# Optimization experiments

Measured on AMD Instinct MI355X. Metric: run time of the kernel, lower is better.

The kernel has to match this reference:

```python
import jax, jax.numpy as jnp
import numpy as np

B, S, D, A, C, TT, T, NS = 64, 512, 1024, 128, 64, 32, 40, 64
NEG = -1e9


def setup_inputs() -> dict:
    key = jax.random.key(0)
    ks = jax.random.split(key, 24)
    n = lambda k, sh, s: jax.random.normal(k, sh, dtype=jnp.float32) * s
    inp = {
        "encoded_src": n(ks[0], (B, S, D), 1.0),
        "encoded_col": n(ks[1], (B, C, D), 1.0),
        "encoded_tab": n(ks[2], (B, TT, D), 1.0),
        "h0": n(ks[3], (B, D), 1.0),
        "c0": n(ks[4], (B, D), 1.0),
        "action_emb": n(ks[5], (A, D), 0.1),
        "symbol_emb": n(ks[6], (NS, D), 0.1),
        "W_tgt": n(ks[7], (D, D), 0.02), "b_tgt": jnp.zeros((D,), jnp.float32),
        "W_act": n(ks[8], (D, D), 0.02), "b_act": jnp.zeros((D,), jnp.float32),
        "W_col": n(ks[9], (D, D), 0.02), "b_col": jnp.zeros((D,), jnp.float32),
        "W_tab": n(ks[10], (D, D), 0.02), "b_tab": jnp.zeros((D,), jnp.float32),
        "W_out": n(ks[11], (D, D), 0.02), "b_out": jnp.zeros((D,), jnp.float32),
        "W_ih": n(ks[12], (3 * D, 4 * D), 0.02), "b_ih": jnp.zeros((4 * D,), jnp.float32),
        "W_hh": n(ks[13], (D, 4 * D), 0.02), "b_hh": jnp.zeros((4 * D,), jnp.float32),
        "src_mask": jnp.zeros((B, S), jnp.int32),
        "col_mask": jnp.zeros((B, C), jnp.int32),
        "tab_mask": jnp.zeros((B, TT), jnp.int32),
        "action_mask": jnp.zeros((B, A), jnp.int32),
        "cur_node_ids": jax.random.randint(ks[14], (T, B), 0, NS, dtype=jnp.int32),
        "kind": jax.random.randint(ks[15], (T, B), 0, 3, dtype=jnp.int32),
        "gold_idx": jax.random.randint(ks[16], (T, B), 0, TT, dtype=jnp.int32),
    }
    return inp


def reference(encoded_src, encoded_col, encoded_tab, h0, c0, action_emb, symbol_emb,
              W_tgt, b_tgt, W_act, b_act, W_col, b_col, W_tab, b_tab, W_out, b_out,
              W_ih, b_ih, W_hh, b_hh,
              src_mask, col_mask, tab_mask, action_mask, cur_node_ids, kind, gold_idx):
    dt = encoded_src.dtype
    nT, nB = cur_node_ids.shape
    nA = action_emb.shape[0]
    nC = encoded_col.shape[1]
    nTT = encoded_tab.shape[1]
    dim = encoded_src.shape[-1]

    # mask==1 means masked-out (matches torch code: allowed positions set to 0)
    src_bias = jnp.where(src_mask == 1, NEG, 0.0).astype(dt)
    act_bias = jnp.where(action_mask == 1, NEG, 0.0).astype(dt)
    col_bias = jnp.where(col_mask == 1, NEG, 0.0).astype(dt)
    tab_bias = jnp.where(tab_mask == 1, NEG, 0.0).astype(dt)

    # previous-action embedding per step: gather from action table / encoded cols / encoded tabs
    bidx = jnp.arange(nB)
    prev_a = action_emb[gold_idx % nA]                       # [T,B,D]
    prev_c = encoded_col[bidx[None, :], gold_idx % nC]       # [T,B,D]
    prev_t = encoded_tab[bidx[None, :], gold_idx % nTT]      # [T,B,D]
    k3 = kind[..., None]
    prev_sel = jnp.where(k3 == 0, prev_a, jnp.where(k3 == 1, prev_c, prev_t))
    # step 0 uses a zero prev-action embedding
    prev_emb = jnp.concatenate([jnp.zeros((1, nB, dim), dt), prev_sel[:-1]], axis=0)
    node_emb = symbol_emb[cur_node_ids]                      # [T,B,D]

    def step(carry, xs):
        h, c, loss = carry
        pe, ne, kd, gi = xs
        # attention over encoded_src using affine(h) as query
        q = h @ W_tgt + b_tgt                                            # [B,D]
        att = jax.nn.softmax(jnp.einsum('bsd,bd->bs', encoded_src, q) + src_bias, axis=-1)
        ctx = jnp.einsum('bs,bsd->bd', att, encoded_src)                 # [B,D]
        # LSTMCell
        x = jnp.concatenate([pe, ne, ctx], axis=-1)                      # [B,3D]
        gates = x @ W_ih + b_ih + h @ W_hh + b_hh                        # [B,4D]
        i, f, g, o = jnp.split(gates, 4, axis=-1)
        c2 = jax.nn.sigmoid(f) * c + jax.nn.sigmoid(i) * jnp.tanh(g)
        h2 = jax.nn.sigmoid(o) * jnp.tanh(c2)
        out = h2 @ W_out + b_out                                         # [B,D]
        # three prediction heads (action / column / table views)
        la = jax.nn.log_softmax(jnp.einsum('ad,bd->ba', action_emb, out @ W_act + b_act) + act_bias, axis=-1)
        lc = jax.nn.log_softmax(jnp.einsum('bcd,bd->bc', encoded_col, out @ W_col + b_col) + col_bias, axis=-1)
        lt = jax.nn.log_softmax(jnp.einsum('btd,bd->bt', encoded_tab, out @ W_tab + b_tab) + tab_bias, axis=-1)
        ga = jnp.take_along_axis(la, (gi % nA)[:, None], 1)[:, 0]
        gc = jnp.take_along_axis(lc, (gi % nC)[:, None], 1)[:, 0]
        gt = jnp.take_along_axis(lt, (gi % nTT)[:, None], 1)[:, 0]
        lp = jnp.where(kd == 0, ga, jnp.where(kd == 1, gc, gt))
        return (h2, c2, loss - lp), None

    (h, c, loss), _ = jax.lax.scan(step, (h0, c0, jnp.zeros((nB,), dt)),
                                   (prev_emb, node_emb, kind, gold_idx))
    return loss
```

## Files before the change

kernel.cpp:

```cpp
#include <hip/hip_runtime.h>
#include <math.h>

typedef short s8v __attribute__((ext_vector_type(8)));
typedef __bf16 bf8 __attribute__((ext_vector_type(8)));
typedef float f4v __attribute__((ext_vector_type(4)));

#define DEV static __device__ __forceinline__

DEV ushort f2bf(float f){
  union { float f; unsigned u; } v; v.f = f;
  unsigned u = v.u;
  return (ushort)((u + 0x7fffu + ((u>>16)&1u)) >> 16);
}
DEV float bf2f(ushort u){
  union { unsigned u; float f; } v; v.u = ((unsigned)u)<<16; return v.f;
}
DEV float sigm(float x){ return 1.0f/(1.0f + __expf(-x)); }
DEV float tanh_(float x){ float e=__expf(2.f*x); return 1.f - 2.f/(e+1.f); }
DEV float wred(float x){
  #pragma unroll
  for(int off=32; off; off>>=1) x += __shfl_xor(x, off, 64);
  return x;
}
DEV int swz(int row, int uscol){
  return (row<<6) + ((((uscol>>3) ^ (row&7))<<3) | (uscol&7));
}
DEV void gload16(const void* g, void* l){
  __builtin_amdgcn_global_load_lds((const __attribute__((address_space(1))) void*)g,
                                   (__attribute__((address_space(3))) void*)l, 16, 0, 0);
}
DEV int gperm(int n){
  return (((n&1023)>>4)<<6) | ((n>>10)<<4) | (n&15);
}


__global__ void k_cast(const float* __restrict__ s, ushort* __restrict__ d, long n4){
  long i = (long)blockIdx.x*256 + threadIdx.x;
  const long st = (long)gridDim.x*256;
  for(; i<n4; i+=st){
    float4 v = ((const float4*)s)[i];
    ushort4 o; o.x=f2bf(v.x); o.y=f2bf(v.y); o.z=f2bf(v.z); o.w=f2bf(v.w);
    ((ushort4*)d)[i]=o;
  }
}

__global__ __launch_bounds__(256) void k_tr7(const float* __restrict__ wih,
    const float* __restrict__ whh, const float* __restrict__ wtgt,
    const float* __restrict__ wcol, const float* __restrict__ wtab,
    const float* __restrict__ wact, ushort* __restrict__ WihT,
    ushort* __restrict__ WcatT, ushort* __restrict__ WtgtT, ushort* __restrict__ BcatT)
{
  __shared__ ushort T[64][72];
  const int bid = blockIdx.x;
  const float* src; ushort* dst; int C, ldd, roff, cx, ry; bool pm;
  if(bid < 2048){ src=wih; C=4096; dst=WihT; ldd=2048; roff=0; cx=bid&63; ry=bid>>6; pm=true; }
  else if(bid < 3072){ int j=bid-2048; src=wih+2048L*4096; C=4096; dst=WcatT; ldd=2048; roff=0; cx=j&63; ry=j>>6; pm=true; }
  else if(bid < 4096){ int j=bid-3072; src=whh; C=4096; dst=WcatT; ldd=2048; roff=1024; cx=j&63; ry=j>>6; pm=true; }
  else if(bid < 4352){ int j=bid-4096; src=wtgt; C=1024; dst=WtgtT; ldd=1024; roff=0; cx=j&15; ry=j>>4; pm=false; }
  else if(bid < 4608){ int j=bid-4352; src=wcol; C=1024; dst=BcatT; ldd=1024; roff=0; cx=j&15; ry=j>>4; pm=false; }
  else if(bid < 4864){ int j=bid-4608; src=wtab; C=1024; dst=BcatT+1048576; ldd=1024; roff=0; cx=j&15; ry=j>>4; pm=false; }
  else { int j=bid-4864; src=wact; C=1024; dst=BcatT+2097152; ldd=1024; roff=0; cx=j&15; ry=j>>4; pm=false; }
  const int c0 = cx<<6, r0 = ry<<6;
  const int tid = threadIdx.x;
  {
    const int rr = tid>>2, cc = (tid&3)<<4;
    const float* s = src + (long)(r0+rr)*C + c0 + cc;
    float4 v0=*(const float4*)(s), v1=*(const float4*)(s+4), v2=*(const float4*)(s+8), v3=*(const float4*)(s+12);
    ushort* t = &T[rr][cc];
    t[0]=f2bf(v0.x); t[1]=f2bf(v0.y); t[2]=f2bf(v0.z); t[3]=f2bf(v0.w);
    t[4]=f2bf(v1.x); t[5]=f2bf(v1.y); t[6]=f2bf(v1.z); t[7]=f2bf(v1.w);
    t[8]=f2bf(v2.x); t[9]=f2bf(v2.y); t[10]=f2bf(v2.z); t[11]=f2bf(v2.w);
    t[12]=f2bf(v3.x); t[13]=f2bf(v3.y); t[14]=f2bf(v3.z); t[15]=f2bf(v3.w);
  }
  __syncthreads();
  {
    const int rr = tid>>2, cc = (tid&3)<<4;
    s8v o0, o1;
    #pragma unroll
    for(int i=0;i<8;i++){ o0[i]=(short)T[cc+i][rr]; o1[i]=(short)T[cc+8+i][rr]; }
    const int n = c0 + rr;
    const int nr = pm ? gperm(n) : n;
    ushort* dp = dst + (long)nr*ldd + roff + r0 + cc;
    *(s8v*)dp = o0; *(s8v*)(dp+8) = o1;
  }
}

__global__ void k_gatherP(const float* __restrict__ emba, const float* __restrict__ ecol,
                          const float* __restrict__ etab, const float* __restrict__ symb,
                          const int* __restrict__ kindv, const int* __restrict__ gold,
                          const int* __restrict__ cur, ushort* __restrict__ P){
  long i = (long)blockIdx.x*256 + threadIdx.x;
  const long st = (long)gridDim.x*256;
  const long n4 = 2560L*2048/4;
  for(; i<n4; i+=st){
    long pos = i*4; int row = (int)(pos>>11); int col = (int)(pos&2047);
    int t = row>>6, b = row&63;
    ushort4 o;
    if(col < 1024){
      if(t==0){ o.x=o.y=o.z=o.w=0; *(ushort4*)&P[pos]=o; continue; }
      int k = kindv[(t-1)*64+b];
      int gi = gold[(t-1)*64+b];
      const float* s;
      if(k==0) s = emba + ((long)(gi & 127))*1024 + col;
      else if(k==1) s = ecol + (((long)b<<6) + (gi & 63))*1024 + col;
      else s = etab + (((long)b<<5) + (gi & 31))*1024 + col;
      float4 v = *(const float4*)s;
      o.x=f2bf(v.x); o.y=f2bf(v.y); o.z=f2bf(v.z); o.w=f2bf(v.w);
    } else {
      const float* s = symb + ((long)cur[t*64+b])*1024 + (col-1024);
      float4 v = *(const float4*)s;
      o.x=f2bf(v.x); o.y=f2bf(v.y); o.z=f2bf(v.z); o.w=f2bf(v.w);
    }
    *(ushort4*)&P[pos] = o;
  }
}

__global__ void k_init(const float* __restrict__ h0, const float* __restrict__ c0,
                       const float* __restrict__ bih, const float* __restrict__ bhh,
                       const int* __restrict__ smask,
                       float* __restrict__ cbuf, ushort* __restrict__ Ab0,
                       float* __restrict__ biasvec, float* __restrict__ sbias){
  int i = blockIdx.x*256 + threadIdx.x;
  if(i < 65536){
    cbuf[i]=c0[i];
    int row=i>>10, col=i&1023;
    Ab0[(row<<11)+1024+col]=f2bf(h0[i]);
  }
  if(i < 32768) sbias[i] = (smask[i]==1) ? -1.0e9f : 0.f;
  if(i < 4096){
    int nt=i>>6, g=(i>>4)&3, j16=i&15;
    int n = (g<<10) | (nt<<4) | j16;
    biasvec[i] = bih[n] + bhh[n];
  }
}

__global__ __launch_bounds__(256) void k_bias1b(const float* __restrict__ bout,
    const ushort* __restrict__ BcatT, const float* __restrict__ ba,
    const float* __restrict__ bc, const float* __restrict__ bt,
    float* __restrict__ vv)
{
  const int wid = blockIdx.x*4 + (threadIdx.x>>6);
  const int l = threadIdx.x & 63;
  const int which = wid>>10, col = wid&1023;
  const ushort* W = (which==0) ? (BcatT + 2097152)
                  : (which==1) ? BcatT
                               : (BcatT + 1048576);
  const float bb = ((which==0)?ba:(which==1)?bc:bt)[col];
  const ushort* wp = W + (long)col*1024 + l*16;
  const float* bp = bout + l*16;
  s8v w0 = *(const s8v*)wp, w1 = *(const s8v*)(wp+8);
  float s = 0.f;
  #pragma unroll
  for(int i=0;i<8;i++){
    s += bf2f((ushort)w0[i]) * bp[i];
    s += bf2f((ushort)w1[i]) * bp[8+i];
  }
  s = wred(s);
  if(l==0) vv[wid] = bb + s;
}

__global__ void k_bias2a(const float* __restrict__ vv, const float* __restrict__ emb,
                         const float* __restrict__ ecol, const float* __restrict__ etab,
                         float* __restrict__ dbuf){
  int wid = blockIdx.x*4 + (threadIdx.x>>6);
  int l = threadIdx.x & 63;
  if(wid >= 6272) return;
  const float* src; const float* v;
  if(wid < 128){ src = emb + ((long)wid<<10); v = vv; }
  else if(wid < 4224){ src = ecol + ((long)(wid-128)<<10); v = vv+1024; }
  else { src = etab + ((long)(wid-4224)<<10); v = vv+2048; }
  const float* sp = src + l*16; const float* vp = v + l*16;
  float s = 0.f;
  #pragma unroll
  for(int i=0;i<16;i+=4){
    float4 a = *(const float4*)(sp+i); float4 bvv = *(const float4*)(vp+i);
    s += a.x*bvv.x + a.y*bvv.y + a.z*bvv.z + a.w*bvv.w;
  }
  s = wred(s);
  if(l==0) dbuf[wid] = s;
}

__global__ void k_bias2b(const float* __restrict__ dbuf,
                         const int* __restrict__ amask, const int* __restrict__ cmask,
                         const int* __restrict__ tmask,
                         float* __restrict__ ca, float* __restrict__ cb, float* __restrict__ ct){
  int i = blockIdx.x*256 + threadIdx.x;
  if(i < 8192){ ca[i] = dbuf[i&127] + ((amask[i]==1)?-1.0e9f:0.f); }
  else if(i < 12288){ int j=i-8192; cb[j] = dbuf[128+j] + ((cmask[j]==1)?-1.0e9f:0.f); }
  else if(i < 14336){ int j=i-12288; ct[j] = dbuf[4224+j] + ((tmask[j]==1)?-1.0e9f:0.f); }
}

template<bool OBF16, bool HASB>
__global__ __launch_bounds__(256,2) void k_gemm128(const ushort* __restrict__ Ap,
    const ushort* __restrict__ Bp, void* __restrict__ Cp, const float* __restrict__ bias,
    int N, int K)
{
  __shared__ __align__(16) ushort As[2][8192];
  __shared__ __align__(16) ushort Bs[2][8192];
  const int tid=threadIdx.x, w=tid>>6, l=tid&63;
  const int wr=w>>1, wc=w&1;
  const int m0=blockIdx.y<<7, n0=blockIdx.x<<7;
  const int lr8 = l>>3, lc = l&7;
  f4v acc[4][4];
  #pragma unroll
  for(int m=0;m<4;m++)
    #pragma unroll
    for(int n=0;n<4;n++) acc[m][n]=(f4v){0.f,0.f,0.f,0.f};

  auto stage=[&](int buf, int k0){
    #pragma unroll
    for(int i=0;i<4;i++){
      const int rb = i*32 + w*8;
      const int row = rb + lr8;
      const int cp = (lc ^ (row&7))<<3;
      gload16(Ap + (long)(m0+row)*K + k0 + cp, &As[buf][rb<<6]);
      gload16(Bp + (long)(n0+row)*K + k0 + cp, &Bs[buf][rb<<6]);
    }
  };
  auto compute=[&](int buf){
    #pragma unroll
    for(int ks=0; ks<2; ks++){
      bf8 av[4], bv[4];
      #pragma unroll
      for(int m=0;m<4;m++){
        const int ar = wr*64 + (m<<4) + (l&15);
        const int ch = (ks<<2) + (l>>4);
        av[m] = *(const bf8*)&As[buf][(ar<<6) + ((ch ^ (ar&7))<<3)];
      }
      #pragma unroll
      for(int n=0;n<4;n++){
        const int br = wc*64 + (n<<4) + (l&15);
        const int ch = (ks<<2) + (l>>4);
        bv[n] = *(const bf8*)&Bs[buf][(br<<6) + ((ch ^ (br&7))<<3)];
      }
      #pragma unroll
      for(int m=0;m<4;m++)
        #pragma unroll
        for(int n=0;n<4;n++)
          acc[m][n] = __builtin_amdgcn_mfma_f32_16x16x32_bf16(av[m], bv[n], acc[m][n], 0,0,0);
    }
  };

  stage(0, 0);
  asm volatile("s_waitcnt vmcnt(0)" ::: "memory");
  __syncthreads();
  int cur=0;
  for(int k0=0;;){
    const int kn = k0+64;
    if(kn<K) stage(cur^1, kn);
    compute(cur);
    asm volatile("s_waitcnt vmcnt(0)" ::: "memory");
    __syncthreads();
    if(kn>=K) break;
    k0=kn; cur^=1;
  }
  #pragma unroll
  for(int m=0;m<4;m++){
    #pragma unroll
    for(int n=0;n<4;n++){
      const int col = n0 + wc*64 + (n<<4) + (l&15);
      float bv_ = 0.f;
      if constexpr(HASB) bv_ = bias[col];
      #pragma unroll
      for(int j=0;j<4;j++){
        const int row = m0 + wr*64 + (m<<4) + ((l>>4)<<2) + j;
        float v = acc[m][n][j] + bv_;
        if constexpr(OBF16) ((ushort*)Cp)[(long)row*N + col] = f2bf(v);
        else ((float*)Cp)[(long)row*N + col] = v;
      }
    }
  }
}

template<bool AF32, bool OBF16, bool HASB>
__global__ __launch_bounds__(256) void k_gemm(const void* __restrict__ Ap,
    const ushort* __restrict__ Bp, void* __restrict__ Cp, const float* __restrict__ bias,
    int M, int N, int K, int lda, int ldb, int ldc, long sAz, long sBz, long sCz)
{
  __shared__ __align__(16) ushort As[4096];
  __shared__ __align__(16) ushort Bs[4096];
  const int tid=threadIdx.x, w=tid>>6, l=tid&63, q4=l>>4;
  const int r=tid>>2, cc=(tid&3)<<4;
  const int m0=blockIdx.y<<6, n0=blockIdx.x<<6;
  const int z=blockIdx.z;
  f4v acc[4];
  #pragma unroll
  for(int i=0;i<4;i++) acc[i]=(f4v){0.f,0.f,0.f,0.f};

  struct PF { float4 f0,f1,f2,f3; s8v u0,u1,b0,b1; };
  PF pA, pB;

  auto loadAB=[&](int k0, PF& p){
    const int gm = m0 + r;
    if constexpr(AF32){
      if(gm < M){
        const float* a = (const float*)Ap + sAz*z + (long)gm*lda + k0 + cc;
        p.f0=*(const float4*)(a); p.f1=*(const float4*)(a+4); p.f2=*(const float4*)(a+8); p.f3=*(const float4*)(a+12);
      } else { p.f0=p.f1=p.f2=p.f3=make_float4(0.f,0.f,0.f,0.f); }
    } else {
      if(gm < M){
        const ushort* a = (const ushort*)Ap + sAz*z + (long)gm*lda + k0 + cc;
        p.u0=*(const s8v*)a; p.u1=*(const s8v*)(a+8);
      } else { p.u0=p.u1=(s8v){0,0,0,0,0,0,0,0}; }
    }
    const ushort* b = Bp + sBz*z + (long)(n0+r)*ldb + k0 + cc;
    p.b0=*(const s8v*)b; p.b1=*(const s8v*)(b+8);
  };
  auto stage=[&](const PF& p){
    s8v a0, a1;
    if constexpr(AF32){
      a0[0]=(short)f2bf(p.f0.x); a0[1]=(short)f2bf(p.f0.y); a0[2]=(short)f2bf(p.f0.z); a0[3]=(short)f2bf(p.f0.w);
      a0[4]=(short)f2bf(p.f1.x); a0[5]=(short)f2bf(p.f1.y); a0[6]=(short)f2bf(p.f1.z); a0[7]=(short)f2bf(p.f1.w);
      a1[0]=(short)f2bf(p.f2.x); a1[1]=(short)f2bf(p.f2.y); a1[2]=(short)f2bf(p.f2.z); a1[3]=(short)f2bf(p.f2.w);
      a1[4]=(short)f2bf(p.f3.x); a1[5]=(short)f2bf(p.f3.y); a1[6]=(short)f2bf(p.f3.z); a1[7]=(short)f2bf(p.f3.w);
    } else { a0=p.u0; a1=p.u1; }
    *(s8v*)&As[swz(r,cc)] = a0; *(s8v*)&As[swz(r,cc+8)] = a1;
    *(s8v*)&Bs[swz(r,cc)] = p.b0; *(s8v*)&Bs[swz(r,cc+8)] = p.b1;
  };
  auto compute=[&](){
    #pragma unroll
    for(int ks=0; ks<64; ks+=32){
      bf8 av = *(const bf8*)&As[swz((w<<4)+(l&15), ks+(q4<<3))];
      #pragma unroll
      for(int nf=0; nf<4; nf++){
        bf8 bv = *(const bf8*)&Bs[swz((nf<<4)+(l&15), ks+(q4<<3))];
        acc[nf] = __builtin_amdgcn_mfma_f32_16x16x32_bf16(av, bv, acc[nf], 0, 0, 0);
      }
    }
  };

  loadAB(0, pA); loadAB(64, pB);
  for(int k0=0; k0<K; k0+=128){
    stage(pA); __syncthreads();
    if(k0+128 < K) loadAB(k0+128, pA);
    compute(); __syncthreads();
    stage(pB); __syncthreads();
    if(k0+192 < K) loadAB(k0+192, pB);
    compute(); __syncthreads();
  }
  #pragma unroll
  for(int nf=0; nf<4; nf++){
    const int col = n0 + (nf<<4) + (l&15);
    float bv = 0.f;
    if constexpr(HASB) bv = bias[col];
    #pragma unroll
    for(int j=0;j<4;j++){
      const int row = m0 + (w<<4) + ((l>>4)<<2) + j;
      if(row < M){
        float v = acc[nf][j] + bv;
        if constexpr(OBF16) ((ushort*)Cp)[sCz*z + (long)row*ldc + col] = f2bf(v);
        else ((float*)Cp)[sCz*z + (long)row*ldc + col] = v;
      }
    }
  }
}


__global__ __launch_bounds__(256) void k_attn(const ushort* __restrict__ esrc,
    const float* __restrict__ q, const float* __restrict__ sbias,
    float* __restrict__ pm, float* __restrict__ pl, float* __restrict__ pctx)
{
  const int b = blockIdx.x>>4, j = blockIdx.x&15;
  const int tid = threadIdx.x, w = tid>>6, l = tid&63;
  __shared__ float ms[4], ls[4];
  __shared__ float ctxs[4][1024];
  float qr[16];
  {
    const float* qp = q + (b<<10) + (l<<4);
    #pragma unroll
    for(int i=0;i<16;i+=4){ float4 v=*(const float4*)(qp+i); qr[i]=v.x; qr[i+1]=v.y; qr[i+2]=v.z; qr[i+3]=v.w; }
  }
  float m = -3.4e38f, lsum = 0.f;
  float cacc[16];
  #pragma unroll
  for(int i=0;i<16;i++) cacc[i]=0.f;
  const int sbase = (j<<5) + w;
  for(int rr=0; rr<8; rr++){
    const int s = sbase + (rr<<2);
    const ushort* ep = esrc + (((long)((b<<9) + s))<<10) + (l<<4);
    s8v e0 = *(const s8v*)ep, e1 = *(const s8v*)(ep+8);
    float ef[16];
    #pragma unroll
    for(int i=0;i<8;i++){ ef[i]=bf2f((ushort)e0[i]); ef[8+i]=bf2f((ushort)e1[i]); }
    float d = 0.f;
    #pragma unroll
    for(int i=0;i<16;i++) d += ef[i]*qr[i];
    d = wred(d);
    d += sbias[(b<<9)+s];
    const float mn = fmaxf(m, d);
    const float sc = __expf(m - mn);
    const float p = __expf(d - mn);
    lsum = lsum*sc + p;
    #pragma unroll
    for(int i=0;i<16;i++) cacc[i] = cacc[i]*sc + p*ef[i];
    m = mn;
  }
  if(l==0){ ms[w]=m; ls[w]=lsum; }
  #pragma unroll
  for(int i=0;i<16;i++) ctxs[w][(l<<4)+i]=cacc[i];
  __syncthreads();
  const float mb = fmaxf(fmaxf(ms[0],ms[1]),fmaxf(ms[2],ms[3]));
  const float w0=__expf(ms[0]-mb), w1=__expf(ms[1]-mb), w2=__expf(ms[2]-mb), w3=__expf(ms[3]-mb);
  const float lb = ls[0]*w0 + ls[1]*w1 + ls[2]*w2 + ls[3]*w3;
  const int jb = (j<<6) + b;
  float* pc = pctx + ((long)jb<<10);
  for(int d0=tid; d0<1024; d0+=256){
    pc[d0] = ctxs[0][d0]*w0 + ctxs[1][d0]*w1 + ctxs[2][d0]*w2 + ctxs[3][d0]*w3;
  }
  if(tid==0){ pm[jb]=mb; pl[jb]=lb; }
}

__global__ __launch_bounds__(256) void k_combine(const float* __restrict__ pm,
    const float* __restrict__ pl, const float* __restrict__ pctx, ushort* __restrict__ Ab)
{
  const int idx = blockIdx.x*256 + threadIdx.x;
  const int b = idx>>7, c0 = (idx&127)<<3;
  float mv[16];
  #pragma unroll
  for(int j=0;j<16;j++) mv[j] = pm[(j<<6)+b];
  float M = mv[0];
  #pragma unroll
  for(int j=1;j<16;j++) M = fmaxf(M, mv[j]);
  float e[16]; float den = 0.f;
  #pragma unroll
  for(int j=0;j<16;j++){ e[j] = __expf(mv[j]-M); den += pl[(j<<6)+b]*e[j]; }
  const float inv = 1.f/den;
  float s0=0,s1=0,s2=0,s3=0,s4=0,s5=0,s6=0,s7=0;
  #pragma unroll
  for(int j=0;j<16;j++){
    const float wj = e[j]*inv;
    const float* p = pctx + (((long)((j<<6)+b))<<10) + c0;
    float4 v0=*(const float4*)p, v1=*(const float4*)(p+4);
    s0+=wj*v0.x; s1+=wj*v0.y; s2+=wj*v0.z; s3+=wj*v0.w;
    s4+=wj*v1.x; s5+=wj*v1.y; s6+=wj*v1.z; s7+=wj*v1.w;
  }
  s8v o;
  o[0]=(short)f2bf(s0); o[1]=(short)f2bf(s1); o[2]=(short)f2bf(s2); o[3]=(short)f2bf(s3);
  o[4]=(short)f2bf(s4); o[5]=(short)f2bf(s5); o[6]=(short)f2bf(s6); o[7]=(short)f2bf(s7);
  *(s8v*)&Ab[(b<<11)+c0] = o;
}

__global__ __launch_bounds__(256) void k_lstm(const ushort* __restrict__ Abuf,
    const float* __restrict__ cin, const ushort* __restrict__ WcatP,
    const ushort* __restrict__ gpre_t, float* __restrict__ cout,
    ushort* __restrict__ AbOut, ushort* __restrict__ h2t)
{
  __shared__ __align__(16) ushort As[4096];
  __shared__ __align__(16) ushort Bs[4096];
  const int tid=threadIdx.x, w=tid>>6, l=tid&63, q4=l>>4, l15=l&15;
  const int r=tid>>2, cc=(tid&3)<<4;
  const int nt = blockIdx.x;
  f4v acc[4];
  #pragma unroll
  for(int nf=0;nf<4;nf++){
    #pragma unroll
    for(int jj=0;jj<4;jj++){
      const int row = (w<<4) + ((l>>4)<<2) + jj;
      acc[nf][jj] = bf2f(gpre_t[((long)row<<12) + (nt<<6) + (nf<<4) + l15]);
    }
  }
  struct PF { s8v a0,a1,b0,b1; };
  PF pA, pB;
  auto loadAB=[&](int k0, PF& p){
    const ushort* a = Abuf + ((long)r<<11) + k0 + cc;
    p.a0=*(const s8v*)a; p.a1=*(const s8v*)(a+8);
    const ushort* bp = WcatP + ((long)((nt<<6)+r)<<11) + k0 + cc;
    p.b0=*(const s8v*)bp; p.b1=*(const s8v*)(bp+8);
  };
  auto stage=[&](const PF& p){
    *(s8v*)&As[swz(r,cc)] = p.a0; *(s8v*)&As[swz(r,cc+8)] = p.a1;
    *(s8v*)&Bs[swz(r,cc)] = p.b0; *(s8v*)&Bs[swz(r,cc+8)] = p.b1;
  };
  auto compute=[&](){
    #pragma unroll
    for(int ks=0; ks<64; ks+=32){
      bf8 av = *(const bf8*)&As[swz((w<<4)+l15, ks+(q4<<3))];
      #pragma unroll
      for(int nf=0;nf<4;nf++){
        bf8 bv = *(const bf8*)&Bs[swz((nf<<4)+l15, ks+(q4<<3))];
        acc[nf] = __builtin_amdgcn_mfma_f32_16x16x32_bf16(av, bv, acc[nf], 0, 0, 0);
      }
    }
  };
  loadAB(0, pA); loadAB(64, pB);
  for(int k0=0; k0<2048; k0+=128){
    stage(pA); __syncthreads();
    if(k0+128 < 2048) loadAB(k0+128, pA);
    compute(); __syncthreads();
    stage(pB); __syncthreads();
    if(k0+192 < 2048) loadAB(k0+192, pB);
    compute(); __syncthreads();
  }
  #pragma unroll
  for(int jj=0;jj<4;jj++){
    const int row = (w<<4) + ((l>>4)<<2) + jj;
    const int j = (nt<<4) + l15;
    const float iv = acc[0][jj], fv = acc[1][jj], gv = acc[2][jj], ov = acc[3][jj];
    const float cold = cin[(row<<10)+j];
    const float c2 = sigm(fv)*cold + sigm(iv)*tanh_(gv);
    const float h2v = sigm(ov)*tanh_(c2);
    cout[(row<<10)+j] = c2;
    const ushort hb = f2bf(h2v);
    AbOut[(row<<11) + 1024 + j] = hb;
    h2t[(row<<10)+j] = hb;
  }
}

__global__ __launch_bounds__(256) void k_loss2(const float* __restrict__ la,
    const float* __restrict__ lcb, const float* __restrict__ ltb,
    const float* __restrict__ ca, const float* __restrict__ cb, const float* __restrict__ ct,
    const int* __restrict__ gold, const int* __restrict__ kindv, float* __restrict__ lossbuf)
{
  const int wv = threadIdx.x>>6, l = threadIdx.x&63;
  const int tb = blockIdx.x*4 + wv;
  const int t = tb>>6, b = tb&63;
  const int kd = kindv[tb];
  const int gi = gold[tb];
  const float* ptr; const float* cons; int R;
  if(kd==0){ ptr = la + (long)tb*128; cons = ca + (b<<7); R=128; }
  else if(kd==1){ ptr = lcb + (long)b*2560 + t*64; cons = cb + (b<<6); R=64; }
  else { ptr = ltb + (long)b*2560 + t*64; cons = ct + (b<<5); R=32; }
  const int gidx = gi & (R-1);
  const float v  = (l < R) ? (ptr[l] + cons[l]) : -3.4e38f;
  const float v2 = (R==128) ? (ptr[l+64] + cons[l+64]) : -3.4e38f;
  float mx = fmaxf(v, v2);
  #pragma unroll
  for(int off=32; off; off>>=1) mx = fmaxf(mx, __shfl_xor(mx, off, 64));
  float s = ((l<R)?__expf(v-mx):0.f) + ((R==128)?__expf(v2-mx):0.f);
  s = wred(s);
  const float gv = ptr[gidx] + cons[gidx];
  if(l==0) lossbuf[tb] = gv - (mx + __logf(s));
}

__global__ void k_loss_fin(const float* __restrict__ lossbuf, float* __restrict__ out){
  int b = threadIdx.x;
  if(b < 64){
    float s = 0.f;
    for(int t=0;t<40;t++) s += lossbuf[(t<<6)+b];
    out[b] = -s;
  }
}


extern "C" void kernel_launch(void* const* d_in, const int* in_sizes, int n_in,
                              void* d_out, int out_size, void* d_ws, size_t ws_size,
                              hipStream_t stream)
{
  const float *e_src=(const float*)d_in[0], *e_col=(const float*)d_in[1], *e_tab=(const float*)d_in[2];
  const float *h0=(const float*)d_in[3], *c0=(const float*)d_in[4];
  const float *emba=(const float*)d_in[5], *embs=(const float*)d_in[6];
  const float *W_tgt=(const float*)d_in[7], *b_tgt=(const float*)d_in[8];
  const float *W_act=(const float*)d_in[9], *b_act=(const float*)d_in[10];
  const float *W_col=(const float*)d_in[11], *b_col=(const float*)d_in[12];
  const float *W_tab=(const float*)d_in[13], *b_tab=(const float*)d_in[14];
  const float *W_out=(const float*)d_in[15], *b_out=(const float*)d_in[16];
  const float *W_ih=(const float*)d_in[17], *b_ih=(const float*)d_in[18];
  const float *W_hh=(const float*)d_in[19], *b_hh=(const float*)d_in[20];
  const int *smask=(const int*)d_in[21], *cmask=(const int*)d_in[22], *tmask=(const int*)d_in[23];
  const int *amask=(const int*)d_in[24];
  const int *cur=(const int*)d_in[25], *kindp=(const int*)d_in[26], *goldp=(const int*)d_in[27];

  char* wp = (char*)d_ws;
  auto alloc = [&](size_t n)->char*{ char* p = wp; wp += (n + 255) & ~(size_t)255; return p; };
  ushort* esrc_bf = (ushort*)alloc(67108864);
  ushort* WihT    = (ushort*)alloc(16777216);
  ushort* WcatP   = (ushort*)alloc(16777216);
  ushort* WtgtT   = (ushort*)alloc(2097152);
  ushort* BcatT   = (ushort*)alloc(6291456);
  ushort* Woutb   = (ushort*)alloc(2097152);
  float*  U       = (float*) alloc(12582912);
  ushort* Ubf     = (ushort*)alloc(6291456);
  ushort* GAt     = (ushort*)alloc(262144);
  ushort* GCt     = (ushort*)alloc(8388608);
  ushort* GTt     = (ushort*)alloc(8388608);
  ushort* gpre    = (ushort*)alloc(20971520);
  float* biasvec  = (float*)alloc(16384);
  float* sbias    = (float*)alloc(131072);
  float* vv       = (float*)alloc(12288);
  float* dbuf     = (float*)alloc(25088);
  float* ca       = (float*)alloc(32768);
  float* cb       = (float*)alloc(16384);
  float* ctb      = (float*)alloc(8192);
  float* pm       = (float*)alloc(4096);
  float* pl       = (float*)alloc(4096);
  float* pctx     = (float*)alloc(4194304);
  ushort* Ab0     = (ushort*)alloc(262144);
  ushort* Ab1     = (ushort*)alloc(262144);
  float* cbuf0    = (float*)alloc(262144);
  float* cbuf1    = (float*)alloc(262144);
  float* qb       = (float*)alloc(262144);
  ushort* h2a     = (ushort*)alloc(5242880);
  float* la       = (float*)alloc(1310720);
  float* lcb      = (float*)alloc(655360);
  float* ltb      = (float*)alloc(655360);
  float* lossbuf  = (float*)alloc(10240);
  ushort* P       = (ushort*)U;
  float* out      = (float*)d_out;

  k_cast<<<4096,256,0,stream>>>(e_src, esrc_bf, 8388608L);
  k_cast<<<512,256,0,stream>>>(W_out, Woutb, 262144L);
  k_tr7<<<5120,256,0,stream>>>(W_ih, W_hh, W_tgt, W_col, W_tab, W_act,
                               WihT, WcatP, WtgtT, BcatT);
  k_init<<<256,256,0,stream>>>(h0, c0, b_ih, b_hh, smask, cbuf0, Ab0, biasvec, sbias);

  { dim3 g(24,8); k_gemm128<false,false><<<g,256,0,stream>>>(Woutb, BcatT, U, nullptr, 3072, 1024); }
  k_cast<<<1024,256,0,stream>>>(U, Ubf, 786432L);
  { dim3 g(16,2); k_gemm<true,true,false><<<g,256,0,stream>>>(emba, Ubf+2048, GAt, nullptr,
        128,1024,1024, 1024,3072,1024, 0,0,0); }
  { dim3 g(16,1,64); k_gemm<true,true,false><<<g,256,0,stream>>>(e_col, Ubf, GCt, nullptr,
        64,1024,1024, 1024,3072,1024, 65536,0,65536); }
  { dim3 g(16,1,64); k_gemm<true,true,false><<<g,256,0,stream>>>(e_tab, Ubf+1024, GTt, nullptr,
        32,1024,1024, 1024,3072,1024, 32768,0,65536); }
  k_bias1b<<<768,256,0,stream>>>(b_out, BcatT, b_act, b_col, b_tab, vv);
  k_bias2a<<<1568,256,0,stream>>>(vv, emba, e_col, e_tab, dbuf);
  k_bias2b<<<56,256,0,stream>>>(dbuf, amask, cmask, tmask, ca, cb, ctb);

  k_gatherP<<<2048,256,0,stream>>>(emba, e_col, e_tab, embs, kindp, goldp, cur, P);
  { dim3 g(32,20); k_gemm128<true,true><<<g,256,0,stream>>>(P, WihT, gpre, biasvec, 4096, 2048); }
  { dim3 g(16,1); k_gemm<true,false,true><<<g,256,0,stream>>>(h0, WtgtT, qb, b_tgt,
        64,1024,1024, 1024,1024,1024, 0,0,0); }

  for(int t=0; t<40; t++){
    ushort* Ain  = (t&1) ? Ab1 : Ab0;
    ushort* Aout = (t&1) ? Ab0 : Ab1;
    float* ci = (t&1) ? cbuf1 : cbuf0;
    float* co = (t&1) ? cbuf0 : cbuf1;
    k_attn<<<1024,256,0,stream>>>(esrc_bf, qb, sbias, pm, pl, pctx);
    k_combine<<<32,256,0,stream>>>(pm, pl, pctx, Ain);
    k_lstm<<<64,256,0,stream>>>(Ain, ci, WcatP, gpre + (long)t*262144, co, Aout, h2a + (long)t*65536);
    { dim3 g(16,1); k_gemm<false,false,true><<<g,256,0,stream>>>(Aout + 1024, WtgtT, qb, b_tgt,
          64,1024,1024, 2048,1024,1024, 0,0,0); }
  }

  { dim3 g(1,20); k_gemm128<false,false><<<g,256,0,stream>>>(h2a, GAt, la, nullptr, 128, 1024); }
  { dim3 g(1,1,64); k_gemm<false,false,false><<<g,256,0,stream>>>(h2a, GCt, lcb, nullptr,
        40,64,1024, 65536,1024,64, 1024,65536,2560); }
  { dim3 g(1,1,64); k_gemm<false,false,false><<<g,256,0,stream>>>(h2a, GTt, ltb, nullptr,
        40,64,1024, 65536,1024,64, 1024,65536,2560); }
  k_loss2<<<640,256,0,stream>>>(la, lcb, ltb, ca, cb, ctb, goldp, kindp, lossbuf);
  k_loss_fin<<<1,64,0,stream>>>(lossbuf, out);
}
```

Measured before the change: 2.083 ms.

## Fuse attention split-combine into LSTM GEMM A-tile staging, widen attention blocks

```diff
diff --git a/kernel.cpp b/kernel.cpp
--- a/kernel.cpp
+++ b/kernel.cpp
@@ -356,14 +356,14 @@
 }
 
 
-__global__ __launch_bounds__(256) void k_attn(const ushort* __restrict__ esrc,
+__global__ __launch_bounds__(1024) void k_attn2(const ushort* __restrict__ esrc,
     const float* __restrict__ q, const float* __restrict__ sbias,
-    float* __restrict__ pm, float* __restrict__ pl, float* __restrict__ pctx)
-{
-  const int b = blockIdx.x>>4, j = blockIdx.x&15;
+    float* __restrict__ pm, float* __restrict__ pl, ushort* __restrict__ pctxh)
+{
+  const int b = blockIdx.x>>2, j = blockIdx.x&3;
   const int tid = threadIdx.x, w = tid>>6, l = tid&63;
-  __shared__ float ms[4], ls[4];
-  __shared__ float ctxs[4][1024];
+  __shared__ float ms[16], ls[16];
+  __shared__ float ctxs[16][1024];
   float qr[16];
   {
     const float* qp = q + (b<<10) + (l<<4);
@@ -374,9 +374,9 @@
   float cacc[16];
   #pragma unroll
   for(int i=0;i<16;i++) cacc[i]=0.f;
-  const int sbase = (j<<5) + w;
+  const int sbase = (j<<7) + (w<<3);
   for(int rr=0; rr<8; rr++){
-    const int s = sbase + (rr<<2);
+    const int s = sbase + rr;
     const ushort* ep = esrc + (((long)((b<<9) + s))<<10) + (l<<4);
     s8v e0 = *(const s8v*)ep, e1 = *(const s8v*)(ep+8);
     float ef[16];
@@ -399,57 +399,45 @@
   #pragma unroll
   for(int i=0;i<16;i++) ctxs[w][(l<<4)+i]=cacc[i];
   __syncthreads();
-  const float mb = fmaxf(fmaxf(ms[0],ms[1]),fmaxf(ms[2],ms[3]));
-  const float w0=__expf(ms[0]-mb), w1=__expf(ms[1]-mb), w2=__expf(ms[2]-mb), w3=__expf(ms[3]-mb);
-  const float lb = ls[0]*w0 + ls[1]*w1 + ls[2]*w2 + ls[3]*w3;
+  float mv[16];
+  #pragma unroll
+  for(int w2=0;w2<16;w2++) mv[w2]=ms[w2];
+  float M = mv[0];
+  #pragma unroll
+  for(int w2=1;w2<16;w2++) M = fmaxf(M, mv[w2]);
+  float den = 0.f;
+  float e[16];
+  #pragma unroll
+  for(int w2=0;w2<16;w2++){ e[w2]=__expf(mv[w2]-M); den += ls[w2]*e[w2]; }
+  const int c = tid;
+  float s = 0.f;
+  #pragma unroll
+  for(int w2=0;w2<16;w2++) s += e[w2]*ctxs[w2][c];
   const int jb = (j<<6) + b;
-  float* pc = pctx + ((long)jb<<10);
-  for(int d0=tid; d0<1024; d0+=256){
-    pc[d0] = ctxs[0][d0]*w0 + ctxs[1][d0]*w1 + ctxs[2][d0]*w2 + ctxs[3][d0]*w3;
-  }
-  if(tid==0){ pm[jb]=mb; pl[jb]=lb; }
-}
-
-__global__ __launch_bounds__(256) void k_combine(const float* __restrict__ pm,
-    const float* __restrict__ pl, const float* __restrict__ pctx, ushort* __restrict__ Ab)
-{
-  const int idx = blockIdx.x*256 + threadIdx.x;
-  const int b = idx>>7, c0 = (idx&127)<<3;
-  float mv[16];
-  #pragma unroll
-  for(int j=0;j<16;j++) mv[j] = pm[(j<<6)+b];
-  float M = mv[0];
-  #pragma unroll
-  for(int j=1;j<16;j++) M = fmaxf(M, mv[j]);
-  float e[16]; float den = 0.f;
-  #pragma unroll
-  for(int j=0;j<16;j++){ e[j] = __expf(mv[j]-M); den += pl[(j<<6)+b]*e[j]; }
-  const float inv = 1.f/den;
-  float s0=0,s1=0,s2=0,s3=0,s4=0,s5=0,s6=0,s7=0;
-  #pragma unroll
-  for(int j=0;j<16;j++){
-    const float wj = e[j]*inv;
-    const float* p = pctx + (((long)((j<<6)+b))<<10) + c0;
-    float4 v0=*(const float4*)p, v1=*(const float4*)(p+4);
-    s0+=wj*v0.x; s1+=wj*v0.y; s2+=wj*v0.z; s3+=wj*v0.w;
-    s4+=wj*v1.x; s5+=wj*v1.y; s6+=wj*v1.z; s7+=wj*v1.w;
-  }
-  s8v o;
-  o[0]=(short)f2bf(s0); o[1]=(short)f2bf(s1); o[2]=(short)f2bf(s2); o[3]=(short)f2bf(s3);
-  o[4]=(short)f2bf(s4); o[5]=(short)f2bf(s5); o[6]=(short)f2bf(s6); o[7]=(short)f2bf(s7);
-  *(s8v*)&Ab[(b<<11)+c0] = o;
-}
-
-__global__ __launch_bounds__(256) void k_lstm(const ushort* __restrict__ Abuf,
+  pctxh[((long)jb<<10)+c] = f2bf(s);
+  if(tid==0){ pm[jb]=M; pl[jb]=den; }
+}
+
+__global__ __launch_bounds__(256) void k_lstm2(const ushort* __restrict__ Abuf,
+    const ushort* __restrict__ pctxh, const float* __restrict__ pm, const float* __restrict__ pl,
     const float* __restrict__ cin, const ushort* __restrict__ WcatP,
     const ushort* __restrict__ gpre_t, float* __restrict__ cout,
     ushort* __restrict__ AbOut, ushort* __restrict__ h2t)
 {
   __shared__ __align__(16) ushort As[4096];
   __shared__ __align__(16) ushort Bs[4096];
+  __shared__ float wjs[4][64];
   const int tid=threadIdx.x, w=tid>>6, l=tid&63, q4=l>>4, l15=l&15;
   const int r=tid>>2, cc=(tid&3)<<4;
   const int nt = blockIdx.x;
+  if(tid < 64){
+    const float m0v=pm[tid], m1v=pm[64+tid], m2v=pm[128+tid], m3v=pm[192+tid];
+    const float mm = fmaxf(fmaxf(m0v,m1v),fmaxf(m2v,m3v));
+    const float e0=__expf(m0v-mm), e1=__expf(m1v-mm), e2=__expf(m2v-mm), e3=__expf(m3v-mm);
+    const float den = pl[tid]*e0 + pl[64+tid]*e1 + pl[128+tid]*e2 + pl[192+tid]*e3;
+    const float inv = 1.0f/den;
+    wjs[0][tid]=e0*inv; wjs[1][tid]=e1*inv; wjs[2][tid]=e2*inv; wjs[3][tid]=e3*inv;
+  }
   f4v acc[4];
   #pragma unroll
   for(int nf=0;nf<4;nf++){
@@ -459,16 +447,40 @@
       acc[nf][jj] = bf2f(gpre_t[((long)row<<12) + (nt<<6) + (nf<<4) + l15]);
     }
   }
-  struct PF { s8v a0,a1,b0,b1; };
+  __syncthreads();
+  struct PF { s8v a0,a1,a2,a3,a4,a5,a6,a7; s8v b0,b1; };
   PF pA, pB;
   auto loadAB=[&](int k0, PF& p){
-    const ushort* a = Abuf + ((long)r<<11) + k0 + cc;
-    p.a0=*(const s8v*)a; p.a1=*(const s8v*)(a+8);
+    if(k0 < 1024){
+      const ushort* p0 = pctxh + ((long)r<<10) + k0 + cc;
+      const ushort* p1 = p0 + 65536;
+      const ushort* p2 = p0 + 131072;
+      const ushort* p3 = p0 + 196608;
+      p.a0=*(const s8v*)p0; p.a1=*(const s8v*)(p0+8);
+      p.a2=*(const s8v*)p1; p.a3=*(const s8v*)(p1+8);
+      p.a4=*(const s8v*)p2; p.a5=*(const s8v*)(p2+8);
+      p.a6=*(const s8v*)p3; p.a7=*(const s8v*)(p3+8);
+    } else {
+      const ushort* a = Abuf + ((long)r<<11) + k0 + cc;
+      p.a0=*(const s8v*)a; p.a1=*(const s8v*)(a+8);
+    }
     const ushort* bp = WcatP + ((long)((nt<<6)+r)<<11) + k0 + cc;
     p.b0=*(const s8v*)bp; p.b1=*(const s8v*)(bp+8);
   };
-  auto stage=[&](const PF& p){
-    *(s8v*)&As[swz(r,cc)] = p.a0; *(s8v*)&As[swz(r,cc+8)] = p.a1;
+  auto stage=[&](const PF& p, int k0){
+    s8v o0, o1;
+    if(k0 < 1024){
+      const float w0=wjs[0][r], w1=wjs[1][r], w2=wjs[2][r], w3=wjs[3][r];
+      #pragma unroll
+      for(int i=0;i<8;i++){
+        float v0 = w0*bf2f((ushort)p.a0[i]) + w1*bf2f((ushort)p.a2[i])
+                 + w2*bf2f((ushort)p.a4[i]) + w3*bf2f((ushort)p.a6[i]);
+        float v1 = w0*bf2f((ushort)p.a1[i]) + w1*bf2f((ushort)p.a3[i])
+                 + w2*bf2f((ushort)p.a5[i]) + w3*bf2f((ushort)p.a7[i]);
+        o0[i]=(short)f2bf(v0); o1[i]=(short)f2bf(v1);
+      }
+    } else { o0=p.a0; o1=p.a1; }
+    *(s8v*)&As[swz(r,cc)] = o0; *(s8v*)&As[swz(r,cc+8)] = o1;
     *(s8v*)&Bs[swz(r,cc)] = p.b0; *(s8v*)&Bs[swz(r,cc+8)] = p.b1;
   };
   auto compute=[&](){
@@ -484,10 +496,10 @@
   };
   loadAB(0, pA); loadAB(64, pB);
   for(int k0=0; k0<2048; k0+=128){
-    stage(pA); __syncthreads();
+    stage(pA, k0); __syncthreads();
     if(k0+128 < 2048) loadAB(k0+128, pA);
     compute(); __syncthreads();
-    stage(pB); __syncthreads();
+    stage(pB, k0+64); __syncthreads();
     if(k0+192 < 2048) loadAB(k0+192, pB);
     compute(); __syncthreads();
   }
@@ -581,9 +593,9 @@
   float* ca       = (float*)alloc(32768);
   float* cb       = (float*)alloc(16384);
   float* ctb      = (float*)alloc(8192);
-  float* pm       = (float*)alloc(4096);
-  float* pl       = (float*)alloc(4096);
-  float* pctx     = (float*)alloc(4194304);
+  float* pm       = (float*)alloc(1024);
+  float* pl       = (float*)alloc(1024);
+  ushort* pctxh   = (ushort*)alloc(524288);
   ushort* Ab0     = (ushort*)alloc(262144);
   ushort* Ab1     = (ushort*)alloc(262144);
   float* cbuf0    = (float*)alloc(262144);
@@ -625,9 +637,9 @@
     ushort* Aout = (t&1) ? Ab0 : Ab1;
     float* ci = (t&1) ? cbuf1 : cbuf0;
     float* co = (t&1) ? cbuf0 : cbuf1;
-    k_attn<<<1024,256,0,stream>>>(esrc_bf, qb, sbias, pm, pl, pctx);
-    k_combine<<<32,256,0,stream>>>(pm, pl, pctx, Ain);
-    k_lstm<<<64,256,0,stream>>>(Ain, ci, WcatP, gpre + (long)t*262144, co, Aout, h2a + (long)t*65536);
+    k_attn2<<<256,1024,0,stream>>>(esrc_bf, qb, sbias, pm, pl, pctxh);
+    k_lstm2<<<64,256,0,stream>>>(Ain, pctxh, pm, pl, ci, WcatP,
+        gpre + (long)t*262144, co, Aout, h2a + (long)t*65536);
     { dim3 g(16,1); k_gemm<false,false,true><<<g,256,0,stream>>>(Aout + 1024, WtgtT, qb, b_tgt,
           64,1024,1024, 2048,1024,1024, 0,0,0); }
   }
```

Result: slower. 2.486 ms (+19.4%).
